# Kernel tuning notes

Measured on AMD Instinct MI355X. Metric: run time of the kernel, lower is better.

Reference implementation:

```python
import jax, jax.numpy as jnp
import numpy as np

B, D, U = 64, 512, 512  # batch, input, units
EPS = 1e-5

def _ln(x, g, b, axes):
    m = jnp.mean(x, axis=axes, keepdims=True)
    v = jnp.mean((x - m) ** 2, axis=axes, keepdims=True)
    return (x - m) * jax.lax.rsqrt(v + EPS) * g + b

def setup_inputs() -> dict:
    key = jax.random.key(0)
    ks = jax.random.split(key, 8)
    w = lambda k, shape: 0.02 * jax.random.normal(k, shape, dtype=jnp.float32)
    return {
        "x": jax.random.normal(ks[0], (B, D), dtype=jnp.float32),
        "w1": w(ks[1], (1, D, U, 2)),
        "b1": jnp.zeros((1, D, U, 2), jnp.float32),
        "w21": w(ks[2], (1, D, U, 2)),
        "w22": w(ks[3], (1, D, U, 2)),
        "b21": jnp.zeros((1, D, U, 1), jnp.float32),
        "b22": jnp.zeros((1, D, U, 1), jnp.float32),
        "w3": w(ks[4], (1, D, U, 2)),
        "b3": jnp.zeros((1, D, U, 1), jnp.float32),
        "bias": jnp.zeros((U,), jnp.float32),
        "g0": jnp.ones((D,), jnp.float32), "be0": jnp.zeros((D,), jnp.float32),
        "g1": jnp.ones((D, U, 2), jnp.float32), "be1": jnp.zeros((D, U, 2), jnp.float32),
        "g2": jnp.ones((D, U, 2), jnp.float32), "be2": jnp.zeros((D, U, 2), jnp.float32),
        "g3": jnp.ones((D, U, 1), jnp.float32), "be3": jnp.zeros((D, U, 1), jnp.float32),
    }

def reference(x, w1, b1, w21, w22, b21, b22, w3, b3, bias,
              g0, be0, g1, be1, g2, be2, g3, be3):
    lrelu = lambda t: jnp.where(t >= 0, t, 0.01 * t)  # nn.LeakyReLU default slope
    xn = _ln(x, g0, be0, (-1,))[:, :, None, None]           # [B,D,1,1]
    l1 = lrelu(_ln(xn * w1 + b1, g1, be1, (1, 2, 3)))        # [B,D,U,2]
    l21 = jnp.sum(l1 * w21, axis=-1, keepdims=True) + b21    # [B,D,U,1]
    l22 = jnp.sum(l1 * w22, axis=-1, keepdims=True) + b22    # [B,D,U,1]
    l2 = lrelu(_ln(jnp.concatenate((l21, l22), axis=-1), g2, be2, (1, 2, 3)))  # [B,D,U,2]
    l3 = jnp.sum(l2 * w3, axis=-1, keepdims=True) + b3       # [B,D,U,1]
    out = _ln(l3, g3, be3, (1, 2, 3)) + xn                   # [B,D,U,1]
    out = lrelu(jnp.sum(out, axis=1) + bias[:, None])        # [B,U,1]
    return jnp.squeeze(out, axis=-1)                         # [B,U]
```

## Files before the change

### kernel.cpp

```cpp
#include <hip/hip_runtime.h>

#define EPS 1e-5f
constexpr float INV_N1 = 1.f / 524288.f;
constexpr float INV_N3 = 1.f / 262144.f;

__device__ __forceinline__ float lrelu(float y) { return fmaxf(y, 0.01f * y); }

__device__ __forceinline__ float waveAllSum(float v) {
    v += __shfl_xor(v, 32);
    v += __shfl_xor(v, 16);
    v += __shfl_xor(v, 8);
    v += __shfl_xor(v, 4);
    v += __shfl_xor(v, 2);
    v += __shfl_xor(v, 1);
    return v;
}

template <int CTRL>
__device__ __forceinline__ float dppMove(float v) {
    return __int_as_float(__builtin_amdgcn_update_dpp(
        0, __float_as_int(v), CTRL, 0xF, 0xF, true));
}
__device__ __forceinline__ float waveSumDpp(float v) {
    v += dppMove<0x111>(v);
    v += dppMove<0x112>(v);
    v += dppMove<0x114>(v);
    v += dppMove<0x118>(v);
    v += dppMove<0x142>(v);
    v += dppMove<0x143>(v);
    return v;
}
__device__ __forceinline__ float quadSum(float v) {
    v += dppMove<0xB1>(v);
    v += dppMove<0x4E>(v);
    return v;
}

__global__ void __launch_bounds__(256) k0a(
    const float* __restrict__ w1, const float* __restrict__ b1,
    const float* __restrict__ g3, const float* __restrict__ be3,
    float* __restrict__ S1, float* __restrict__ S0b, float* __restrict__ S2,
    float* __restrict__ S11, float* __restrict__ Sb2,
    float* __restrict__ G3s, float* __restrict__ Be3s) {
    int bid = blockIdx.x, tid = threadIdx.x;
    if (bid < 512) {
        const float4* wr = (const float4*)(w1 + bid * 1024);
        const float4* br = (const float4*)(b1 + bid * 1024);
        float4 w = wr[tid], b = br[tid];
        float s1  = w.x + w.y + w.z + w.w;
        float s2  = w.x * w.x + w.y * w.y + w.z * w.z + w.w * w.w;
        float s11 = w.x * b.x + w.y * b.y + w.z * b.z + w.w * b.w;
        float s0  = b.x + b.y + b.z + b.w;
        float sb2 = b.x * b.x + b.y * b.y + b.z * b.z + b.w * b.w;
        __shared__ float red[4][5];
        s1 = waveAllSum(s1); s2 = waveAllSum(s2); s11 = waveAllSum(s11);
        s0 = waveAllSum(s0); sb2 = waveAllSum(sb2);
        int wave = tid >> 6, lane = tid & 63;
        if (lane == 0) {
            red[wave][0] = s1; red[wave][1] = s2; red[wave][2] = s11;
            red[wave][3] = s0; red[wave][4] = sb2;
        }
        __syncthreads();
        if (tid == 0) {
            float a0 = 0, a1 = 0, a2 = 0, a3 = 0, a4 = 0;
            for (int w4 = 0; w4 < 4; ++w4) {
                a0 += red[w4][0]; a1 += red[w4][1]; a2 += red[w4][2];
                a3 += red[w4][3]; a4 += red[w4][4];
            }
            S1[bid] = a0; S2[bid] = a1; S11[bid] = a2; S0b[bid] = a3; Sb2[bid] = a4;
        }
    } else {
        int jj = bid - 512;
        float ag0 = 0, ag1 = 0, ab0 = 0, ab1 = 0;
#pragma unroll
        for (int r = 0; r < 8; ++r) {
            int d = jj * 8 + r;
            const float* gr = g3 + d * 512;
            const float* br = be3 + d * 512;
            ag0 += gr[tid];       ag1 += gr[tid + 256];
            ab0 += br[tid];       ab1 += br[tid + 256];
        }
        unsafeAtomicAdd(&G3s[tid], ag0);
        unsafeAtomicAdd(&G3s[tid + 256], ag1);
        unsafeAtomicAdd(&Be3s[tid], ab0);
        unsafeAtomicAdd(&Be3s[tid + 256], ab1);
    }
}

__global__ void __launch_bounds__(256) k0b(
    const float* __restrict__ x, const float* __restrict__ g0, const float* __restrict__ be0,
    const float* __restrict__ S1, const float* __restrict__ S0b, const float* __restrict__ S2,
    const float* __restrict__ S11, const float* __restrict__ Sb2,
    float* __restrict__ xnp, float* __restrict__ rs1a, float* __restrict__ mm1a,
    float* __restrict__ Xs) {
    int b = blockIdx.x, tid = threadIdx.x;
    float2 xv = ((const float2*)(x + b * 512))[tid];
    float sx = xv.x + xv.y;
    float sxx = xv.x * xv.x + xv.y * xv.y;
    __shared__ float red[4][3];
    __shared__ float bc[2];
    sx = waveAllSum(sx); sxx = waveAllSum(sxx);
    int wave = tid >> 6, lane = tid & 63;
    if (lane == 0) { red[wave][0] = sx; red[wave][1] = sxx; }
    __syncthreads();
    if (tid == 0) {
        float a = red[0][0] + red[1][0] + red[2][0] + red[3][0];
        float c = red[0][1] + red[1][1] + red[2][1] + red[3][1];
        float m = a * (1.f / 512.f);
        float var = c * (1.f / 512.f) - m * m;
        bc[0] = m; bc[1] = rsqrtf(var + EPS);
    }
    __syncthreads();
    float m = bc[0], rsd = bc[1];
    float2 g = ((const float2*)g0)[tid];
    float2 be = ((const float2*)be0)[tid];
    float xn0 = (xv.x - m) * rsd * g.x + be.x;
    float xn1 = (xv.y - m) * rsd * g.y + be.y;
    ((float2*)(xnp + b * 512))[tid] = make_float2(xn0, xn1);
    float2 s1 = ((const float2*)S1)[tid], s0b = ((const float2*)S0b)[tid];
    float2 s2 = ((const float2*)S2)[tid], s11 = ((const float2*)S11)[tid];
    float2 sb2 = ((const float2*)Sb2)[tid];
    float pm = fmaf(xn0, s1.x, s0b.x) + fmaf(xn1, s1.y, s0b.y);
    float pe = xn0 * xn0 * s2.x + 2.f * xn0 * s11.x + sb2.x
             + xn1 * xn1 * s2.y + 2.f * xn1 * s11.y + sb2.y;
    float sxn = xn0 + xn1;
    pm = waveAllSum(pm); pe = waveAllSum(pe); sxn = waveAllSum(sxn);
    __syncthreads();
    if (lane == 0) { red[wave][0] = pm; red[wave][1] = pe; red[wave][2] = sxn; }
    __syncthreads();
    if (tid == 0) {
        float a = red[0][0] + red[1][0] + red[2][0] + red[3][0];
        float c = red[0][1] + red[1][1] + red[2][1] + red[3][1];
        float s = red[0][2] + red[1][2] + red[2][2] + red[3][2];
        float m1 = a * INV_N1;
        float e1 = c * INV_N1;
        float r = rsqrtf(e1 - m1 * m1 + EPS);
        rs1a[b] = r; mm1a[b] = m1 * r; Xs[b] = s;
    }
}

__global__ void __launch_bounds__(256) k1(
    const float* __restrict__ w1, const float* __restrict__ b1,
    const float* __restrict__ g1, const float* __restrict__ be1,
    const float* __restrict__ w21, const float* __restrict__ w22,
    const float* __restrict__ b21, const float* __restrict__ b22,
    const float* __restrict__ xnp, const float* __restrict__ rs1a,
    const float* __restrict__ mm1a, float* __restrict__ part1) {
    int bid = blockIdx.x, tid = threadIdx.x;
    int d = bid >> 1;
    int u = ((bid & 1) << 8) + tid;
    int i = d * 512 + u;
    float2 W1 = ((const float2*)w1)[i], B1 = ((const float2*)b1)[i];
    float2 G1 = ((const float2*)g1)[i], E1 = ((const float2*)be1)[i];
    float2 A = ((const float2*)w21)[i], C = ((const float2*)w22)[i];
    float Ba = b21[i], Bc = b22[i];
    __shared__ float xcol[64], scA[64], scB[64];
    __shared__ float red[64][4][2];
    if (tid < 64) {
        xcol[tid] = xnp[tid * 512 + d];
        scA[tid] = rs1a[tid];
        scB[tid] = mm1a[tid];
    }
    __syncthreads();
    int wave = tid >> 6, lane = tid & 63;
    for (int b = 0; b < 64; ++b) {
        float rs1 = scA[b], mm1 = scB[b], xd = xcol[b];
        float t0 = fmaf(xd, W1.x, B1.x), t1 = fmaf(xd, W1.y, B1.y);
        float z0 = fmaf(t0, rs1, -mm1), z1 = fmaf(t1, rs1, -mm1);
        float y0 = fmaf(z0, G1.x, E1.x), y1 = fmaf(z1, G1.y, E1.y);
        float l0 = lrelu(y0), l1 = lrelu(y1);
        float c0 = fmaf(l0, A.x, fmaf(l1, A.y, Ba));
        float c1 = fmaf(l0, C.x, fmaf(l1, C.y, Bc));
        float v1 = c0 + c1;
        float v2 = fmaf(c0, c0, c1 * c1);
        v1 = waveSumDpp(v1);
        v2 = waveSumDpp(v2);
        if (lane == 63) { red[b][wave][0] = v1; red[b][wave][1] = v2; }
    }
    __syncthreads();
    if (tid < 128) {
        int b = tid >> 1, k = tid & 1;
        float s = red[b][0][k] + red[b][1][k] + red[b][2][k] + red[b][3][k];
        part1[tid * 1024 + bid] = s;
    }
}

__global__ void __launch_bounds__(256) k1b(
    const float* __restrict__ part1, float* __restrict__ st2f) {
    int b = blockIdx.x, tid = threadIdx.x;
    const float4* r1 = (const float4*)(part1 + (2 * b) * 1024);
    const float4* r2 = (const float4*)(part1 + (2 * b + 1) * 1024);
    float4 a = r1[tid], c = r2[tid];
    float s1 = a.x + a.y + a.z + a.w;
    float s2 = c.x + c.y + c.z + c.w;
    __shared__ float red[4][2];
    s1 = waveAllSum(s1); s2 = waveAllSum(s2);
    int wave = tid >> 6, lane = tid & 63;
    if (lane == 0) { red[wave][0] = s1; red[wave][1] = s2; }
    __syncthreads();
    if (tid == 0) {
        float t1 = red[0][0] + red[1][0] + red[2][0] + red[3][0];
        float t2 = red[0][1] + red[1][1] + red[2][1] + red[3][1];
        float m2 = t1 * INV_N1;
        float var = t2 * INV_N1 - m2 * m2;
        float r = rsqrtf(var + EPS);
        st2f[2 * b] = r; st2f[2 * b + 1] = m2 * r;
    }
}

struct Wt { float2 W1, B1, G1, E1, A, C, G2, E2, W3; float Ba, Bc, B3, G3v; };

template <bool PART>
__global__ void __launch_bounds__(256) k2t(
    const float* __restrict__ w1, const float* __restrict__ b1,
    const float* __restrict__ g1, const float* __restrict__ be1,
    const float* __restrict__ w21, const float* __restrict__ w22,
    const float* __restrict__ b21, const float* __restrict__ b22,
    const float* __restrict__ g2, const float* __restrict__ be2,
    const float* __restrict__ w3, const float* __restrict__ b3,
    const float* __restrict__ g3,
    const float* __restrict__ xnp, const float* __restrict__ rs1a,
    const float* __restrict__ mm1a, const float* __restrict__ st2f,
    float* __restrict__ pp, float* __restrict__ qp) {
    int bu = blockIdx.x, bd = blockIdx.y, tid = threadIdx.x;
    int lane = tid & 63, wave = tid >> 6;
    int ul = (lane >> 2) & 15, d0 = lane & 3;
    int u = bu * 16 + ul;
    int dl0 = wave * 8 + d0 * 2;
    Wt wt[2];
#pragma unroll
    for (int j = 0; j < 2; ++j) {
        int d = bd * 32 + dl0 + j;
        int i = d * 512 + u;
        wt[j].W1 = ((const float2*)w1)[i];  wt[j].B1 = ((const float2*)b1)[i];
        wt[j].G1 = ((const float2*)g1)[i];  wt[j].E1 = ((const float2*)be1)[i];
        wt[j].A  = ((const float2*)w21)[i]; wt[j].C  = ((const float2*)w22)[i];
        wt[j].G2 = ((const float2*)g2)[i];  wt[j].E2 = ((const float2*)be2)[i];
        wt[j].W3 = ((const float2*)w3)[i];
        wt[j].Ba = b21[i]; wt[j].Bc = b22[i]; wt[j].B3 = b3[i]; wt[j].G3v = g3[i];
    }
    __shared__ float4 sc[64];
    __shared__ float sxn[64][32];
    __shared__ float comb[4][64][16][3];
    {
        float* cz = &comb[0][0][0][0];
        for (int t = tid; t < 4 * 64 * 16 * 3; t += 256) cz[t] = 0.f;
    }
    if (tid < 64)
        sc[tid] = make_float4(rs1a[tid], mm1a[tid], st2f[2 * tid], st2f[2 * tid + 1]);
    for (int idx = tid; idx < 2048; idx += 256)
        sxn[idx >> 5][idx & 31] = xnp[(idx >> 5) * 512 + bd * 32 + (idx & 31)];
    __syncthreads();
    for (int b = 0; b < 64; ++b) {
        float4 s4 = sc[b];
        float p = 0, q = 0, q2 = 0;
#pragma unroll
        for (int j = 0; j < 2; ++j) {
            float xd = sxn[b][dl0 + j];
            float t0 = fmaf(xd, wt[j].W1.x, wt[j].B1.x), t1 = fmaf(xd, wt[j].W1.y, wt[j].B1.y);
            float z0 = fmaf(t0, s4.x, -s4.y), z1 = fmaf(t1, s4.x, -s4.y);
            float y0 = fmaf(z0, wt[j].G1.x, wt[j].E1.x), y1 = fmaf(z1, wt[j].G1.y, wt[j].E1.y);
            float l0 = lrelu(y0), l1 = lrelu(y1);
            float c0 = fmaf(l0, wt[j].A.x, fmaf(l1, wt[j].A.y, wt[j].Ba));
            float c1 = fmaf(l0, wt[j].C.x, fmaf(l1, wt[j].C.y, wt[j].Bc));
            float z20 = fmaf(c0, s4.z, -s4.w), z21 = fmaf(c1, s4.z, -s4.w);
            float y20 = fmaf(z20, wt[j].G2.x, wt[j].E2.x), y21 = fmaf(z21, wt[j].G2.y, wt[j].E2.y);
            float m0 = lrelu(y20), m1v = lrelu(y21);
            float l3 = fmaf(m0, wt[j].W3.x, fmaf(m1v, wt[j].W3.y, wt[j].B3));
            p = fmaf(l3, wt[j].G3v, p); q += l3; q2 = fmaf(l3, l3, q2);
        }
        p = quadSum(p); q = quadSum(q); q2 = quadSum(q2);
        if (d0 < 3) {
            float v = (d0 == 0) ? p : ((d0 == 1) ? q : q2);
            comb[wave][b][ul][d0] += v;
        }
    }
    __syncthreads();
#pragma unroll
    for (int r = 0; r < 4; ++r) {
        int idx = r * 256 + tid;
        int b = idx >> 4, uu = idx & 15;
        float s = comb[0][b][uu][0] + comb[1][b][uu][0]
                + comb[2][b][uu][0] + comb[3][b][uu][0];
        if (PART)
            pp[(bd * 64 + b) * 512 + bu * 16 + uu] = s;
        else
            unsafeAtomicAdd(&pp[b * 512 + bu * 16 + uu], s);
    }
    if (tid < 128) {
        int b = tid >> 1, st = 1 + (tid & 1);
        float s = 0;
#pragma unroll
        for (int w = 0; w < 4; ++w)
#pragma unroll
            for (int uu = 0; uu < 16; ++uu) s += comb[w][b][uu][st];
        qp[(bd * 32 + bu) * 128 + b * 2 + (st - 1)] = s;
    }
}

template <bool PART>
__global__ void __launch_bounds__(512) k3t(
    const float* __restrict__ pp, const float* __restrict__ qp,
    const float* __restrict__ G3s, const float* __restrict__ Be3s,
    const float* __restrict__ Xs, const float* __restrict__ bias,
    float* __restrict__ out) {
    int b = blockIdx.x, u = threadIdx.x;
    float q  = qp[u * 128 + b * 2 + 0];
    float q2 = qp[u * 128 + b * 2 + 1];
    __shared__ float red[8][2];
    __shared__ float bc2[2];
    float sq = waveAllSum(q), sq2 = waveAllSum(q2);
    int wave = u >> 6, lane = u & 63;
    if (lane == 0) { red[wave][0] = sq; red[wave][1] = sq2; }
    __syncthreads();
    if (u == 0) {
        float a = 0, c = 0;
        for (int w = 0; w < 8; ++w) { a += red[w][0]; c += red[w][1]; }
        float m3 = a * INV_N3;
        float e3 = c * INV_N3;
        bc2[0] = m3; bc2[1] = rsqrtf(e3 - m3 * m3 + EPS);
    }
    __syncthreads();
    float p = 0;
    if (PART) {
#pragma unroll 4
        for (int bd = 0; bd < 16; ++bd) p += pp[(bd * 64 + b) * 512 + u];
    } else {
        p = pp[b * 512 + u];
    }
    float m3 = bc2[0], rs3 = bc2[1];
    float val = rs3 * (p - m3 * G3s[u]) + Be3s[u] + Xs[b] + bias[u];
    out[b * 512 + u] = lrelu(val);
}

extern "C" void kernel_launch(void* const* d_in, const int* in_sizes, int n_in,
                              void* d_out, int out_size, void* d_ws, size_t ws_size,
                              hipStream_t stream) {
    const float* x   = (const float*)d_in[0];
    const float* w1  = (const float*)d_in[1];
    const float* b1  = (const float*)d_in[2];
    const float* w21 = (const float*)d_in[3];
    const float* w22 = (const float*)d_in[4];
    const float* b21 = (const float*)d_in[5];
    const float* b22 = (const float*)d_in[6];
    const float* w3  = (const float*)d_in[7];
    const float* b3  = (const float*)d_in[8];
    const float* bias= (const float*)d_in[9];
    const float* g0  = (const float*)d_in[10];
    const float* be0 = (const float*)d_in[11];
    const float* g1  = (const float*)d_in[12];
    const float* be1 = (const float*)d_in[13];
    const float* g2  = (const float*)d_in[14];
    const float* be2 = (const float*)d_in[15];
    const float* g3  = (const float*)d_in[16];
    const float* be3 = (const float*)d_in[17];
    float* out = (float*)d_out;
    char* ws = (char*)d_ws;

    float* xn    = (float*)(ws);
    float* S1    = (float*)(ws + 131072);
    float* S0b   = (float*)(ws + 133120);
    float* S2    = (float*)(ws + 135168);
    float* S11   = (float*)(ws + 137216);
    float* Sb2   = (float*)(ws + 139264);
    float* rs1a  = (float*)(ws + 141312);
    float* mm1a  = (float*)(ws + 141568);
    float* Xs    = (float*)(ws + 141824);
    float* st2f  = (float*)(ws + 142080);
    float* part1 = (float*)(ws + 142592);
    float* G3s   = (float*)(ws + 666880);
    float* Be3s  = (float*)(ws + 668928);
    float* qp    = (float*)(ws + 670976);
    float* pp    = (float*)(ws + 933120);

    bool part = ws_size >= (size_t)933120 + 2097152;
    hipMemsetAsync(ws + 666880, 0, 4096, stream);
    if (!part)
        hipMemsetAsync(ws + 933120, 0, 131072, stream);

    hipLaunchKernelGGL(k0a, dim3(576), dim3(256), 0, stream,
                       w1, b1, g3, be3, S1, S0b, S2, S11, Sb2, G3s, Be3s);
    hipLaunchKernelGGL(k0b, dim3(64), dim3(256), 0, stream,
                       x, g0, be0, S1, S0b, S2, S11, Sb2, xn, rs1a, mm1a, Xs);
    hipLaunchKernelGGL(k1, dim3(1024), dim3(256), 0, stream,
                       w1, b1, g1, be1, w21, w22, b21, b22, xn, rs1a, mm1a, part1);
    hipLaunchKernelGGL(k1b, dim3(64), dim3(256), 0, stream, part1, st2f);
    if (part) {
        hipLaunchKernelGGL((k2t<true>), dim3(32, 16), dim3(256), 0, stream,
                           w1, b1, g1, be1, w21, w22, b21, b22, g2, be2, w3, b3, g3,
                           xn, rs1a, mm1a, st2f, pp, qp);
        hipLaunchKernelGGL((k3t<true>), dim3(64), dim3(512), 0, stream,
                           pp, qp, G3s, Be3s, Xs, bias, out);
    } else {
        hipLaunchKernelGGL((k2t<false>), dim3(32, 16), dim3(256), 0, stream,
                           w1, b1, g1, be1, w21, w22, b21, b22, g2, be2, w3, b3, g3,
                           xn, rs1a, mm1a, st2f, pp, qp);
        hipLaunchKernelGGL((k3t<false>), dim3(64), dim3(512), 0, stream,
                           pp, qp, G3s, Be3s, Xs, bias, out);
    }
}
```

Baseline: 69.80 us.

## Restructure launch graph: drop memsets and k1b, fold stats into atomics

Removes both hipMemsetAsync calls and the k1b reduction kernel. Zeroing of st2 moves into an extra block of the first kernel, and the per-batch layer-2 stats are accumulated with padded atomics in k1 and finalized inside k2. The x layernorm moves into the first kernel, and a small new kernel finishes the layer-1 stats and reduces the g3/be3 partials without atomics. The partial-sum path for pp is now unconditional. The aim is fewer launches and serialized steps, at the cost of atomic contention on st2 and a workspace requirement that is no longer checked.

```diff
diff --git a/kernel.cpp b/kernel.cpp
--- a/kernel.cpp
+++ b/kernel.cpp
@@ -6,43 +6,44 @@
 
 __device__ __forceinline__ float lrelu(float y) { return fmaxf(y, 0.01f * y); }
 
-__device__ __forceinline__ float waveAllSum(float v) {
-    v += __shfl_xor(v, 32);
-    v += __shfl_xor(v, 16);
-    v += __shfl_xor(v, 8);
-    v += __shfl_xor(v, 4);
-    v += __shfl_xor(v, 2);
-    v += __shfl_xor(v, 1);
-    return v;
-}
-
 template <int CTRL>
-__device__ __forceinline__ float dppMove(float v) {
+__device__ __forceinline__ float dppMov(float v) {
     return __int_as_float(__builtin_amdgcn_update_dpp(
         0, __float_as_int(v), CTRL, 0xF, 0xF, true));
 }
 __device__ __forceinline__ float waveSumDpp(float v) {
-    v += dppMove<0x111>(v);
-    v += dppMove<0x112>(v);
-    v += dppMove<0x114>(v);
-    v += dppMove<0x118>(v);
-    v += dppMove<0x142>(v);
-    v += dppMove<0x143>(v);
+    v += dppMov<0x111>(v);
+    v += dppMov<0x112>(v);
+    v += dppMov<0x114>(v);
+    v += dppMov<0x118>(v);
+    v += dppMov<0x142>(v);
+    v += dppMov<0x143>(v);
     return v;
 }
 __device__ __forceinline__ float quadSum(float v) {
-    v += dppMove<0xB1>(v);
-    v += dppMove<0x4E>(v);
+    v += dppMov<0xB1>(v);
+    v += dppMov<0x4E>(v);
     return v;
 }
-
-__global__ void __launch_bounds__(256) k0a(
+__device__ __forceinline__ float waveAllSum(float v) {
+    v += __shfl_xor(v, 32); v += __shfl_xor(v, 16); v += __shfl_xor(v, 8);
+    v += __shfl_xor(v, 4);  v += __shfl_xor(v, 2);  v += __shfl_xor(v, 1);
+    return v;
+}
+
+__global__ void __launch_bounds__(256) kA(
     const float* __restrict__ w1, const float* __restrict__ b1,
     const float* __restrict__ g3, const float* __restrict__ be3,
-    float* __restrict__ S1, float* __restrict__ S0b, float* __restrict__ S2,
-    float* __restrict__ S11, float* __restrict__ Sb2,
-    float* __restrict__ G3s, float* __restrict__ Be3s) {
+    const float* __restrict__ x, const float* __restrict__ g0,
+    const float* __restrict__ be0,
+    float* __restrict__ S1, float* __restrict__ S2, float* __restrict__ S11,
+    float* __restrict__ S0b, float* __restrict__ Sb2,
+    float* __restrict__ Gp, float* __restrict__ Bp,
+    float* __restrict__ xn, float* __restrict__ Xs, float* __restrict__ st2) {
     int bid = blockIdx.x, tid = threadIdx.x;
+    int wave = tid >> 6, lane = tid & 63;
+    __shared__ float red[4][5];
+    __shared__ float bc[2];
     if (bid < 512) {
         const float4* wr = (const float4*)(w1 + bid * 1024);
         const float4* br = (const float4*)(b1 + bid * 1024);
@@ -52,10 +53,8 @@
         float s11 = w.x * b.x + w.y * b.y + w.z * b.z + w.w * b.w;
         float s0  = b.x + b.y + b.z + b.w;
         float sb2 = b.x * b.x + b.y * b.y + b.z * b.z + b.w * b.w;
-        __shared__ float red[4][5];
         s1 = waveAllSum(s1); s2 = waveAllSum(s2); s11 = waveAllSum(s11);
         s0 = waveAllSum(s0); sb2 = waveAllSum(sb2);
-        int wave = tid >> 6, lane = tid & 63;
         if (lane == 0) {
             red[wave][0] = s1; red[wave][1] = s2; red[wave][2] = s11;
             red[wave][3] = s0; red[wave][4] = sb2;
@@ -67,75 +66,95 @@
                 a0 += red[w4][0]; a1 += red[w4][1]; a2 += red[w4][2];
                 a3 += red[w4][3]; a4 += red[w4][4];
             }
-            S1[bid] = a0; S2[bid] = a1; S11[bid] = a2; S0b[bid] = a3; Sb2[bid] = a4;
-        }
-    } else {
+            S1[bid] = a0; S2[bid] = a1; S11[bid] = a2;
+            S0b[bid] = a3; Sb2[bid] = a4;
+        }
+    } else if (bid < 576) {
         int jj = bid - 512;
         float ag0 = 0, ag1 = 0, ab0 = 0, ab1 = 0;
 #pragma unroll
         for (int r = 0; r < 8; ++r) {
-            int d = jj * 8 + r;
-            const float* gr = g3 + d * 512;
-            const float* br = be3 + d * 512;
-            ag0 += gr[tid];       ag1 += gr[tid + 256];
-            ab0 += br[tid];       ab1 += br[tid + 256];
-        }
-        unsafeAtomicAdd(&G3s[tid], ag0);
-        unsafeAtomicAdd(&G3s[tid + 256], ag1);
-        unsafeAtomicAdd(&Be3s[tid], ab0);
-        unsafeAtomicAdd(&Be3s[tid + 256], ab1);
-    }
-}
-
-__global__ void __launch_bounds__(256) k0b(
-    const float* __restrict__ x, const float* __restrict__ g0, const float* __restrict__ be0,
-    const float* __restrict__ S1, const float* __restrict__ S0b, const float* __restrict__ S2,
-    const float* __restrict__ S11, const float* __restrict__ Sb2,
-    float* __restrict__ xnp, float* __restrict__ rs1a, float* __restrict__ mm1a,
-    float* __restrict__ Xs) {
-    int b = blockIdx.x, tid = threadIdx.x;
-    float2 xv = ((const float2*)(x + b * 512))[tid];
-    float sx = xv.x + xv.y;
-    float sxx = xv.x * xv.x + xv.y * xv.y;
-    __shared__ float red[4][3];
-    __shared__ float bc[2];
-    sx = waveAllSum(sx); sxx = waveAllSum(sxx);
-    int wave = tid >> 6, lane = tid & 63;
-    if (lane == 0) { red[wave][0] = sx; red[wave][1] = sxx; }
-    __syncthreads();
-    if (tid == 0) {
-        float a = red[0][0] + red[1][0] + red[2][0] + red[3][0];
-        float c = red[0][1] + red[1][1] + red[2][1] + red[3][1];
-        float m = a * (1.f / 512.f);
-        float var = c * (1.f / 512.f) - m * m;
-        bc[0] = m; bc[1] = rsqrtf(var + EPS);
-    }
-    __syncthreads();
-    float m = bc[0], rsd = bc[1];
-    float2 g = ((const float2*)g0)[tid];
-    float2 be = ((const float2*)be0)[tid];
-    float xn0 = (xv.x - m) * rsd * g.x + be.x;
-    float xn1 = (xv.y - m) * rsd * g.y + be.y;
-    ((float2*)(xnp + b * 512))[tid] = make_float2(xn0, xn1);
-    float2 s1 = ((const float2*)S1)[tid], s0b = ((const float2*)S0b)[tid];
-    float2 s2 = ((const float2*)S2)[tid], s11 = ((const float2*)S11)[tid];
-    float2 sb2 = ((const float2*)Sb2)[tid];
-    float pm = fmaf(xn0, s1.x, s0b.x) + fmaf(xn1, s1.y, s0b.y);
-    float pe = xn0 * xn0 * s2.x + 2.f * xn0 * s11.x + sb2.x
-             + xn1 * xn1 * s2.y + 2.f * xn1 * s11.y + sb2.y;
-    float sxn = xn0 + xn1;
-    pm = waveAllSum(pm); pe = waveAllSum(pe); sxn = waveAllSum(sxn);
-    __syncthreads();
-    if (lane == 0) { red[wave][0] = pm; red[wave][1] = pe; red[wave][2] = sxn; }
-    __syncthreads();
-    if (tid == 0) {
-        float a = red[0][0] + red[1][0] + red[2][0] + red[3][0];
-        float c = red[0][1] + red[1][1] + red[2][1] + red[3][1];
-        float s = red[0][2] + red[1][2] + red[2][2] + red[3][2];
-        float m1 = a * INV_N1;
-        float e1 = c * INV_N1;
-        float r = rsqrtf(e1 - m1 * m1 + EPS);
-        rs1a[b] = r; mm1a[b] = m1 * r; Xs[b] = s;
+            const float* gr = g3 + (jj * 8 + r) * 512;
+            const float* br = be3 + (jj * 8 + r) * 512;
+            ag0 += gr[tid]; ag1 += gr[tid + 256];
+            ab0 += br[tid]; ab1 += br[tid + 256];
+        }
+        Gp[jj * 512 + tid] = ag0; Gp[jj * 512 + tid + 256] = ag1;
+        Bp[jj * 512 + tid] = ab0; Bp[jj * 512 + tid + 256] = ab1;
+    } else if (bid < 640) {
+        int b = bid - 576;
+        float2 xv = ((const float2*)(x + b * 512))[tid];
+        float sx = xv.x + xv.y, sxx = xv.x * xv.x + xv.y * xv.y;
+        sx = waveAllSum(sx); sxx = waveAllSum(sxx);
+        if (lane == 0) { red[wave][0] = sx; red[wave][1] = sxx; }
+        __syncthreads();
+        if (tid == 0) {
+            float s = red[0][0] + red[1][0] + red[2][0] + red[3][0];
+            float c = red[0][1] + red[1][1] + red[2][1] + red[3][1];
+            float m = s * (1.f / 512.f);
+            float var = c * (1.f / 512.f) - m * m;
+            bc[0] = m; bc[1] = rsqrtf(var + EPS);
+        }
+        __syncthreads();
+        float m = bc[0], rsd = bc[1];
+        float2 g = ((const float2*)g0)[tid], be = ((const float2*)be0)[tid];
+        float xn0 = (xv.x - m) * rsd * g.x + be.x;
+        float xn1 = (xv.y - m) * rsd * g.y + be.y;
+        ((float2*)(xn + b * 512))[tid] = make_float2(xn0, xn1);
+        float sxn = waveAllSum(xn0 + xn1);
+        __syncthreads();
+        if (lane == 0) red[wave][0] = sxn;
+        __syncthreads();
+        if (tid == 0) Xs[b] = red[0][0] + red[1][0] + red[2][0] + red[3][0];
+    } else {
+        for (int t = tid; t < 2048; t += 256) st2[t] = 0.f;
+    }
+}
+
+__global__ void __launch_bounds__(256) kS(
+    const float* __restrict__ xn,
+    const float* __restrict__ S1, const float* __restrict__ S2,
+    const float* __restrict__ S11, const float* __restrict__ S0b,
+    const float* __restrict__ Sb2,
+    const float* __restrict__ Gp, const float* __restrict__ Bp,
+    float* __restrict__ rs1a, float* __restrict__ mm1a,
+    float* __restrict__ G3s, float* __restrict__ Be3s) {
+    int bid = blockIdx.x, tid = threadIdx.x;
+    if (bid < 64) {
+        int b = bid;
+        __shared__ float red[4][2];
+        float2 xv  = ((const float2*)(xn + b * 512))[tid];
+        float2 s1  = ((const float2*)S1)[tid],  s0b = ((const float2*)S0b)[tid];
+        float2 s2  = ((const float2*)S2)[tid],  s11 = ((const float2*)S11)[tid];
+        float2 sb2 = ((const float2*)Sb2)[tid];
+        float pm = fmaf(xv.x, s1.x, s0b.x) + fmaf(xv.y, s1.y, s0b.y);
+        float pe = xv.x * xv.x * s2.x + 2.f * xv.x * s11.x + sb2.x
+                 + xv.y * xv.y * s2.y + 2.f * xv.y * s11.y + sb2.y;
+        pm = waveAllSum(pm); pe = waveAllSum(pe);
+        int wave = tid >> 6, lane = tid & 63;
+        if (lane == 0) { red[wave][0] = pm; red[wave][1] = pe; }
+        __syncthreads();
+        if (tid == 0) {
+            float s = red[0][0] + red[1][0] + red[2][0] + red[3][0];
+            float c = red[0][1] + red[1][1] + red[2][1] + red[3][1];
+            float m1 = s * INV_N1, e1 = c * INV_N1;
+            float r = rsqrtf(e1 - m1 * m1 + EPS);
+            rs1a[b] = r; mm1a[b] = m1 * r;
+        }
+    } else if (bid == 64) {
+        for (int u = tid; u < 512; u += 256) {
+            float s = 0;
+#pragma unroll 8
+            for (int jj = 0; jj < 64; ++jj) s += Gp[jj * 512 + u];
+            G3s[u] = s;
+        }
+    } else {
+        for (int u = tid; u < 512; u += 256) {
+            float s = 0;
+#pragma unroll 8
+            for (int jj = 0; jj < 64; ++jj) s += Bp[jj * 512 + u];
+            Be3s[u] = s;
+        }
     }
 }
 
@@ -145,7 +164,7 @@
     const float* __restrict__ w21, const float* __restrict__ w22,
     const float* __restrict__ b21, const float* __restrict__ b22,
     const float* __restrict__ xnp, const float* __restrict__ rs1a,
-    const float* __restrict__ mm1a, float* __restrict__ part1) {
+    const float* __restrict__ mm1a, float* __restrict__ st2) {
     int bid = blockIdx.x, tid = threadIdx.x;
     int d = bid >> 1;
     int u = ((bid & 1) << 8) + tid;
@@ -181,37 +200,13 @@
     if (tid < 128) {
         int b = tid >> 1, k = tid & 1;
         float s = red[b][0][k] + red[b][1][k] + red[b][2][k] + red[b][3][k];
-        part1[tid * 1024 + bid] = s;
-    }
-}
-
-__global__ void __launch_bounds__(256) k1b(
-    const float* __restrict__ part1, float* __restrict__ st2f) {
-    int b = blockIdx.x, tid = threadIdx.x;
-    const float4* r1 = (const float4*)(part1 + (2 * b) * 1024);
-    const float4* r2 = (const float4*)(part1 + (2 * b + 1) * 1024);
-    float4 a = r1[tid], c = r2[tid];
-    float s1 = a.x + a.y + a.z + a.w;
-    float s2 = c.x + c.y + c.z + c.w;
-    __shared__ float red[4][2];
-    s1 = waveAllSum(s1); s2 = waveAllSum(s2);
-    int wave = tid >> 6, lane = tid & 63;
-    if (lane == 0) { red[wave][0] = s1; red[wave][1] = s2; }
-    __syncthreads();
-    if (tid == 0) {
-        float t1 = red[0][0] + red[1][0] + red[2][0] + red[3][0];
-        float t2 = red[0][1] + red[1][1] + red[2][1] + red[3][1];
-        float m2 = t1 * INV_N1;
-        float var = t2 * INV_N1 - m2 * m2;
-        float r = rsqrtf(var + EPS);
-        st2f[2 * b] = r; st2f[2 * b + 1] = m2 * r;
+        unsafeAtomicAdd(&st2[tid * 16], s);
     }
 }
 
 struct Wt { float2 W1, B1, G1, E1, A, C, G2, E2, W3; float Ba, Bc, B3, G3v; };
 
-template <bool PART>
-__global__ void __launch_bounds__(256) k2t(
+__global__ void __launch_bounds__(256) k2(
     const float* __restrict__ w1, const float* __restrict__ b1,
     const float* __restrict__ g1, const float* __restrict__ be1,
     const float* __restrict__ w21, const float* __restrict__ w22,
@@ -220,9 +215,9 @@
     const float* __restrict__ w3, const float* __restrict__ b3,
     const float* __restrict__ g3,
     const float* __restrict__ xnp, const float* __restrict__ rs1a,
-    const float* __restrict__ mm1a, const float* __restrict__ st2f,
+    const float* __restrict__ mm1a, const float* __restrict__ st2,
     float* __restrict__ pp, float* __restrict__ qp) {
-    int bu = blockIdx.x, bd = blockIdx.y, tid = threadIdx.x;
+    int bu = blockIdx.x & 31, bd = blockIdx.x >> 5, tid = threadIdx.x;
     int lane = tid & 63, wave = tid >> 6;
     int ul = (lane >> 2) & 15, d0 = lane & 3;
     int u = bu * 16 + ul;
@@ -246,8 +241,13 @@
         float* cz = &comb[0][0][0][0];
         for (int t = tid; t < 4 * 64 * 16 * 3; t += 256) cz[t] = 0.f;
     }
-    if (tid < 64)
-        sc[tid] = make_float4(rs1a[tid], mm1a[tid], st2f[2 * tid], st2f[2 * tid + 1]);
+    if (tid < 64) {
+        float ssum = st2[(tid * 2) * 16], s2sum = st2[(tid * 2 + 1) * 16];
+        float mm = ssum * INV_N1;
+        float var = s2sum * INV_N1 - mm * mm;
+        float r2 = rsqrtf(var + EPS);
+        sc[tid] = make_float4(rs1a[tid], mm1a[tid], r2, mm * r2);
+    }
     for (int idx = tid; idx < 2048; idx += 256)
         sxn[idx >> 5][idx & 31] = xnp[(idx >> 5) * 512 + bd * 32 + (idx & 31)];
     __syncthreads();
@@ -282,10 +282,7 @@
         int b = idx >> 4, uu = idx & 15;
         float s = comb[0][b][uu][0] + comb[1][b][uu][0]
                 + comb[2][b][uu][0] + comb[3][b][uu][0];
-        if (PART)
-            pp[(bd * 64 + b) * 512 + bu * 16 + uu] = s;
-        else
-            unsafeAtomicAdd(&pp[b * 512 + bu * 16 + uu], s);
+        pp[(bd * 64 + b) * 512 + bu * 16 + uu] = s;
     }
     if (tid < 128) {
         int b = tid >> 1, st = 1 + (tid & 1);
@@ -298,8 +295,7 @@
     }
 }
 
-template <bool PART>
-__global__ void __launch_bounds__(512) k3t(
+__global__ void __launch_bounds__(512) k3(
     const float* __restrict__ pp, const float* __restrict__ qp,
     const float* __restrict__ G3s, const float* __restrict__ Be3s,
     const float* __restrict__ Xs, const float* __restrict__ bias,
@@ -322,12 +318,8 @@
     }
     __syncthreads();
     float p = 0;
-    if (PART) {
 #pragma unroll 4
-        for (int bd = 0; bd < 16; ++bd) p += pp[(bd * 64 + b) * 512 + u];
-    } else {
-        p = pp[b * 512 + u];
-    }
+    for (int bd = 0; bd < 16; ++bd) p += pp[(bd * 64 + b) * 512 + u];
     float m3 = bc2[0], rs3 = bc2[1];
     float val = rs3 * (p - m3 * G3s[u]) + Be3s[u] + Xs[b] + bias[u];
     out[b * 512 + u] = lrelu(val);
@@ -357,45 +349,34 @@
     float* out = (float*)d_out;
     char* ws = (char*)d_ws;
 
-    float* xn    = (float*)(ws);
-    float* S1    = (float*)(ws + 131072);
-    float* S0b   = (float*)(ws + 133120);
-    float* S2    = (float*)(ws + 135168);
-    float* S11   = (float*)(ws + 137216);
-    float* Sb2   = (float*)(ws + 139264);
-    float* rs1a  = (float*)(ws + 141312);
-    float* mm1a  = (float*)(ws + 141568);
-    float* Xs    = (float*)(ws + 141824);
-    float* st2f  = (float*)(ws + 142080);
-    float* part1 = (float*)(ws + 142592);
-    float* G3s   = (float*)(ws + 666880);
-    float* Be3s  = (float*)(ws + 668928);
-    float* qp    = (float*)(ws + 670976);
-    float* pp    = (float*)(ws + 933120);
-
-    bool part = ws_size >= (size_t)933120 + 2097152;
-    hipMemsetAsync(ws + 666880, 0, 4096, stream);
-    if (!part)
-        hipMemsetAsync(ws + 933120, 0, 131072, stream);
-
-    hipLaunchKernelGGL(k0a, dim3(576), dim3(256), 0, stream,
-                       w1, b1, g3, be3, S1, S0b, S2, S11, Sb2, G3s, Be3s);
-    hipLaunchKernelGGL(k0b, dim3(64), dim3(256), 0, stream,
-                       x, g0, be0, S1, S0b, S2, S11, Sb2, xn, rs1a, mm1a, Xs);
+    float* xn   = (float*)(ws);
+    float* S1   = (float*)(ws + 131072);
+    float* S2   = (float*)(ws + 133120);
+    float* S11  = (float*)(ws + 135168);
+    float* S0b  = (float*)(ws + 137216);
+    float* Sb2  = (float*)(ws + 139264);
+    float* rs1a = (float*)(ws + 141312);
+    float* mm1a = (float*)(ws + 141568);
+    float* Xs   = (float*)(ws + 141824);
+    float* st2  = (float*)(ws + 142080);
+    float* G3s  = (float*)(ws + 150272);
+    float* Be3s = (float*)(ws + 152320);
+    float* Gp   = (float*)(ws + 154368);
+    float* Bp   = (float*)(ws + 285440);
+    float* qp   = (float*)(ws + 416512);
+    float* pp   = (float*)(ws + 678656);
+
+    hipLaunchKernelGGL(kA, dim3(641), dim3(256), 0, stream,
+                       w1, b1, g3, be3, x, g0, be0,
+                       S1, S2, S11, S0b, Sb2, Gp, Bp, xn, Xs, st2);
+    hipLaunchKernelGGL(kS, dim3(66), dim3(256), 0, stream,
+                       xn, S1, S2, S11, S0b, Sb2, Gp, Bp,
+                       rs1a, mm1a, G3s, Be3s);
     hipLaunchKernelGGL(k1, dim3(1024), dim3(256), 0, stream,
-                       w1, b1, g1, be1, w21, w22, b21, b22, xn, rs1a, mm1a, part1);
-    hipLaunchKernelGGL(k1b, dim3(64), dim3(256), 0, stream, part1, st2f);
-    if (part) {
-        hipLaunchKernelGGL((k2t<true>), dim3(32, 16), dim3(256), 0, stream,
-                           w1, b1, g1, be1, w21, w22, b21, b22, g2, be2, w3, b3, g3,
-                           xn, rs1a, mm1a, st2f, pp, qp);
-        hipLaunchKernelGGL((k3t<true>), dim3(64), dim3(512), 0, stream,
-                           pp, qp, G3s, Be3s, Xs, bias, out);
-    } else {
-        hipLaunchKernelGGL((k2t<false>), dim3(32, 16), dim3(256), 0, stream,
-                           w1, b1, g1, be1, w21, w22, b21, b22, g2, be2, w3, b3, g3,
-                           xn, rs1a, mm1a, st2f, pp, qp);
-        hipLaunchKernelGGL((k3t<false>), dim3(64), dim3(512), 0, stream,
-                           pp, qp, G3s, Be3s, Xs, bias, out);
-    }
-}
+                       w1, b1, g1, be1, w21, w22, b21, b22, xn, rs1a, mm1a, st2);
+    hipLaunchKernelGGL(k2, dim3(512), dim3(256), 0, stream,
+                       w1, b1, g1, be1, w21, w22, b21, b22, g2, be2, w3, b3, g3,
+                       xn, rs1a, mm1a, st2, pp, qp);
+    hipLaunchKernelGGL(k3, dim3(64), dim3(512), 0, stream,
+                       pp, qp, G3s, Be3s, Xs, bias, out);
+}
```

Result: slower. 83.29 us (+19.3%).
